# Kernel optimization log

Measured on AMD Instinct MI355X. Metric: run time of the kernel, lower is better.

## Reference

```python
import jax, jax.numpy as jnp
import numpy as np

SHORT_LEN = 10
NEG_INF = -1.0e9


def _attn_pool(values, user, w, w_bias, extra_b, mask, softmax_axis):
    # values: [B,L,D], user: [B,D]; linear+bias+relu, dot with user, masked softmax, weighted sum
    h = jax.nn.relu(jnp.einsum('bld,ed->ble', values, w) + w_bias + extra_b)
    s = jnp.einsum('bld,bd->bl', h, user)
    s = jnp.where(mask, NEG_INF, s)
    a = jax.nn.softmax(s, axis=softmax_axis)
    return jnp.einsum('bld,bl->bd', values, a)


def setup_inputs() -> dict:
    key = jax.random.key(0)
    ks = jax.random.split(key, 10)
    B, L, D, NI, NU = 2048, 50, 64, 100000, 100000
    return {
        'seq': jax.random.randint(ks[0], (B, L), 0, NI),
        'user_id': jax.random.randint(ks[1], (B,), 0, NU),
        'item_emb': jax.random.normal(ks[2], (NI, D), jnp.float32) * 0.01,
        'user_emb': jax.random.normal(ks[3], (NU, D), jnp.float32) * 0.01,
        'long_w': jax.random.normal(ks[4], (D, D), jnp.float32) * 0.1,
        'long_w_bias': jax.random.normal(ks[5], (D,), jnp.float32) * 0.1,
        'long_b': jax.random.normal(ks[6], (D,), jnp.float32) * 0.1,
        'long_short_w': jax.random.normal(ks[7], (D, D), jnp.float32) * 0.1,
        'long_short_w_bias': jax.random.normal(ks[8], (D,), jnp.float32) * 0.1,
        'long_short_b': jax.random.normal(ks[9], (D,), jnp.float32) * 0.1,
    }


def reference(seq, user_id, item_emb, user_emb, long_w, long_w_bias, long_b,
              long_short_w, long_short_w_bias, long_short_b):
    e = item_emb[seq]                     # [B,L,D]
    u = user_emb[user_id]                 # [B,D]
    mask = seq == 0                       # padding mask
    # long-term attention pooling (softmax over dim=1)
    long_term = _attn_pool(e, u, long_w, long_w_bias, long_b, mask, 1)[:, None, :]  # [B,1,D]
    # concat long-term summary with last SHORT_LEN items
    short = e[:, -SHORT_LEN:, :]
    mask_ls = jnp.concatenate([jnp.zeros((seq.shape[0], 1), bool), mask[:, -SHORT_LEN:]], axis=1)
    ls = jnp.concatenate([long_term, short], axis=1)  # [B,1+K,D]
    pooled = _attn_pool(ls, u, long_short_w, long_short_w_bias, long_short_b, mask_ls, -1)  # [B,D]
    scores = pooled @ item_emb.T          # [B, n_items]
    return scores
```

## Files before the change

kernel.cpp:

```cpp
#include <hip/hip_runtime.h>
#include <hip/hip_bf16.h>


#define L_SEQ 50
#define D_EMB 64
#define SHORT_LEN 10
#define LS_LEN 11
#define NEG_INF_F (-1000000000.0f)

typedef __bf16 bf16x8 __attribute__((ext_vector_type(8)));
typedef float f32x4 __attribute__((ext_vector_type(4)));

__device__ __forceinline__ float wave_sum(float v) {
#pragma unroll
  for (int off = 32; off > 0; off >>= 1) v += __shfl_xor(v, off, 64);
  return v;
}
__device__ __forceinline__ float wave_max(float v) {
#pragma unroll
  for (int off = 32; off > 0; off >>= 1) v = fmaxf(v, __shfl_xor(v, off, 64));
  return v;
}

__global__ __launch_bounds__(64) void pool_kernel(
    const int* __restrict__ seq, const int* __restrict__ user_id,
    const float* __restrict__ item_emb, const float* __restrict__ user_emb,
    const float* __restrict__ w1, const float* __restrict__ w1b, const float* __restrict__ b1,
    const float* __restrict__ w2, const float* __restrict__ w2b, const float* __restrict__ b2,
    float* __restrict__ pooled_f32, __bf16* __restrict__ pooled_bf) {
  const int b = blockIdx.x;
  const int lane = threadIdx.x;

  __shared__ float e_lds[L_SEQ][D_EMB];
  __shared__ float ls_lds[LS_LEN][D_EMB];
  __shared__ float a_lds[D_EMB];
  __shared__ int seq_lds[L_SEQ];

  if (lane < L_SEQ) seq_lds[lane] = seq[b * L_SEQ + lane];
  const float u = user_emb[(long)user_id[b] * D_EMB + lane];
  __syncthreads();

  for (int l = 0; l < L_SEQ; ++l) {
    e_lds[l][lane] = item_emb[(long)seq_lds[l] * D_EMB + lane];
  }

  float4 w1r[16];
#pragma unroll
  for (int k = 0; k < 16; ++k) w1r[k] = *(const float4*)&w1[lane * D_EMB + 4 * k];
  const float bias1 = w1b[lane] + b1[lane];
  __syncthreads();

  float s_val = 0.0f;
  for (int l = 0; l < L_SEQ; ++l) {
    float acc = bias1;
#pragma unroll
    for (int k = 0; k < 16; ++k) {
      float4 ev = *(const float4*)&e_lds[l][4 * k];
      acc = fmaf(ev.x, w1r[k].x, acc);
      acc = fmaf(ev.y, w1r[k].y, acc);
      acc = fmaf(ev.z, w1r[k].z, acc);
      acc = fmaf(ev.w, w1r[k].w, acc);
    }
    acc = fmaxf(acc, 0.0f);
    float t = wave_sum(acc * u);
    if (lane == l) s_val = (seq_lds[l] == 0) ? NEG_INF_F : t;
  }
  {
    float x = (lane < L_SEQ) ? s_val : -INFINITY;
    float m = wave_max(x);
    float p = (lane < L_SEQ) ? __expf(x - m) : 0.0f;
    float ps = wave_sum(p);
    a_lds[lane] = p / ps;
  }
  __syncthreads();

  float lt = 0.0f;
  for (int l = 0; l < L_SEQ; ++l) lt = fmaf(a_lds[l], e_lds[l][lane], lt);
  __syncthreads();

  ls_lds[0][lane] = lt;
#pragma unroll
  for (int j = 1; j < LS_LEN; ++j)
    ls_lds[j][lane] = e_lds[L_SEQ - SHORT_LEN + (j - 1)][lane];

  float4 w2r[16];
#pragma unroll
  for (int k = 0; k < 16; ++k) w2r[k] = *(const float4*)&w2[lane * D_EMB + 4 * k];
  const float bias2 = w2b[lane] + b2[lane];
  __syncthreads();

  float s2_val = 0.0f;
  for (int j = 0; j < LS_LEN; ++j) {
    float acc = bias2;
#pragma unroll
    for (int k = 0; k < 16; ++k) {
      float4 lv = *(const float4*)&ls_lds[j][4 * k];
      acc = fmaf(lv.x, w2r[k].x, acc);
      acc = fmaf(lv.y, w2r[k].y, acc);
      acc = fmaf(lv.z, w2r[k].z, acc);
      acc = fmaf(lv.w, w2r[k].w, acc);
    }
    acc = fmaxf(acc, 0.0f);
    float t = wave_sum(acc * u);
    bool msk = (j == 0) ? false : (seq_lds[L_SEQ - SHORT_LEN + (j - 1)] == 0);
    if (lane == j) s2_val = msk ? NEG_INF_F : t;
  }
  {
    float x = (lane < LS_LEN) ? s2_val : -INFINITY;
    float m = wave_max(x);
    float p = (lane < LS_LEN) ? __expf(x - m) : 0.0f;
    float ps = wave_sum(p);
    __syncthreads();
    a_lds[lane] = p / ps;
  }
  __syncthreads();

  float po = 0.0f;
#pragma unroll
  for (int j = 0; j < LS_LEN; ++j) po = fmaf(a_lds[j], ls_lds[j][lane], po);
  if (pooled_f32) pooled_f32[(long)b * D_EMB + lane] = po;
  if (pooled_bf) pooled_bf[(long)b * D_EMB + lane] = (__bf16)po;
}

__global__ __launch_bounds__(256) void cvt_bf16_kernel(
    const float* __restrict__ in, __bf16* __restrict__ out, int n8) {
  int i = blockIdx.x * blockDim.x + threadIdx.x;
  if (i >= n8) return;
  float4 a = ((const float4*)in)[2 * i];
  float4 b = ((const float4*)in)[2 * i + 1];
  bf16x8 v;
  v[0] = (__bf16)a.x; v[1] = (__bf16)a.y; v[2] = (__bf16)a.z; v[3] = (__bf16)a.w;
  v[4] = (__bf16)b.x; v[5] = (__bf16)b.y; v[6] = (__bf16)b.z; v[7] = (__bf16)b.w;
  ((bf16x8*)out)[i] = v;
}

__global__ __launch_bounds__(256) void scores_mfma_kernel(
    const __bf16* __restrict__ pooled_bf,
    const __bf16* __restrict__ item_bf,
    float* __restrict__ out, int NI, int n_tiles) {
  const int tid = threadIdx.x;
  const int w = tid >> 6;
  const int l = tid & 63;
  const int lr = l & 15;
  const int lg = l >> 4;
  const int b0 = blockIdx.x * 64;

  bf16x8 afrag[4][2];
#pragma unroll
  for (int g = 0; g < 4; ++g) {
    const __bf16* arow = pooled_bf + (size_t)(b0 + 16 * g + lr) * D_EMB + 8 * lg;
    afrag[g][0] = *(const bf16x8*)(arow);
    afrag[g][1] = *(const bf16x8*)(arow + 32);
  }

  const int t0 = blockIdx.y * 32;
  for (int tl = w; tl < 32; tl += 4) {
    const int t = t0 + tl;
    if (t >= n_tiles) break;
    const __bf16* brow = item_bf + (size_t)(t * 16 + lr) * D_EMB + 8 * lg;
    bf16x8 bf0 = *(const bf16x8*)(brow);
    bf16x8 bf1 = *(const bf16x8*)(brow + 32);
#pragma unroll
    for (int g = 0; g < 4; ++g) {
      f32x4 acc = {0.f, 0.f, 0.f, 0.f};
      acc = __builtin_amdgcn_mfma_f32_16x16x32_bf16(afrag[g][0], bf0, acc, 0, 0, 0);
      acc = __builtin_amdgcn_mfma_f32_16x16x32_bf16(afrag[g][1], bf1, acc, 0, 0, 0);
      float* orow = out + (size_t)(b0 + 16 * g + 4 * lg) * NI + t * 16 + lr;
#pragma unroll
      for (int r = 0; r < 4; ++r) orow[(size_t)r * NI] = acc[r];
    }
  }
}

__global__ __launch_bounds__(256) void scores_kernel(
    const float* __restrict__ pooled, const float* __restrict__ item_emb,
    float* __restrict__ out, int NI) {
  constexpr int STR = 68;
  __shared__ __align__(16) float poolT[64 * STR];
  __shared__ __align__(16) float itemT[64 * STR];

  const int tid = threadIdx.x;
  const int lane = tid & 63;
  const int b0 = blockIdx.x * 64;
  const int i0 = blockIdx.y * 64;

  for (int r = tid >> 6; r < 64; r += 4) {
    poolT[lane * STR + r] = pooled[(long)(b0 + r) * D_EMB + lane];
    int i = i0 + r;
    itemT[lane * STR + r] = (i < NI) ? item_emb[(long)i * D_EMB + lane] : 0.0f;
  }
  __syncthreads();

  const int tx = tid & 15;
  const int ty = tid >> 4;
  float acc[4][4] = {};

#pragma unroll 8
  for (int d = 0; d < 64; ++d) {
    float4 pv = *(const float4*)&poolT[d * STR + ty * 4];
    float4 iv = *(const float4*)&itemT[d * STR + tx * 4];
    float pva[4] = {pv.x, pv.y, pv.z, pv.w};
    float iva[4] = {iv.x, iv.y, iv.z, iv.w};
#pragma unroll
    for (int m = 0; m < 4; ++m)
#pragma unroll
      for (int n = 0; n < 4; ++n) acc[m][n] = fmaf(pva[m], iva[n], acc[m][n]);
  }

  const int ibase = i0 + tx * 4;
  const long orow = (long)(b0 + ty * 4);
  if (i0 + 63 < NI) {
#pragma unroll
    for (int m = 0; m < 4; ++m) {
      float4 v = make_float4(acc[m][0], acc[m][1], acc[m][2], acc[m][3]);
      *(float4*)&out[(orow + m) * (long)NI + ibase] = v;
    }
  } else {
#pragma unroll
    for (int m = 0; m < 4; ++m)
#pragma unroll
      for (int n = 0; n < 4; ++n)
        if (ibase + n < NI) out[(orow + m) * (long)NI + ibase + n] = acc[m][n];
  }
}

extern "C" void kernel_launch(void* const* d_in, const int* in_sizes, int n_in,
                              void* d_out, int out_size, void* d_ws, size_t ws_size,
                              hipStream_t stream) {
  const int* seq = (const int*)d_in[0];
  const int* user_id = (const int*)d_in[1];
  const float* item_emb = (const float*)d_in[2];
  const float* user_emb = (const float*)d_in[3];
  const float* w1 = (const float*)d_in[4];
  const float* w1b = (const float*)d_in[5];
  const float* b1 = (const float*)d_in[6];
  const float* w2 = (const float*)d_in[7];
  const float* w2b = (const float*)d_in[8];
  const float* b2 = (const float*)d_in[9];
  float* out = (float*)d_out;

  const int B = in_sizes[1];
  const int NI = in_sizes[2] / D_EMB;

  const size_t item_bf_bytes = (size_t)NI * D_EMB * 2;
  const size_t pooled_bf_bytes = (size_t)B * D_EMB * 2;
  const bool mfma_ok = (ws_size >= item_bf_bytes + pooled_bf_bytes) &&
                       (NI % 16 == 0) && (B % 64 == 0) && (D_EMB == 64);

  if (mfma_ok) {
    __bf16* item_bf = (__bf16*)d_ws;
    __bf16* pooled_bf = (__bf16*)((char*)d_ws + item_bf_bytes);

    const int n8 = NI * D_EMB / 8;
    cvt_bf16_kernel<<<(n8 + 255) / 256, 256, 0, stream>>>(item_emb, item_bf, n8);

    pool_kernel<<<B, 64, 0, stream>>>(seq, user_id, item_emb, user_emb,
                                      w1, w1b, b1, w2, w2b, b2,
                                      (float*)nullptr, pooled_bf);

    const int n_tiles = NI / 16;
    dim3 grid(B / 64, (n_tiles + 31) / 32);
    scores_mfma_kernel<<<grid, 256, 0, stream>>>(pooled_bf, item_bf, out, NI, n_tiles);
  } else {
    float* pooled = (float*)d_ws;
    pool_kernel<<<B, 64, 0, stream>>>(seq, user_id, item_emb, user_emb,
                                      w1, w1b, b1, w2, w2b, b2,
                                      pooled, (__bf16*)nullptr);
    dim3 grid(B / 64, (NI + 63) / 64);
    scores_kernel<<<grid, 256, 0, stream>>>(pooled, item_emb, out, NI);
  }
}
```

Measured before the change: 313.0 us.

## Fuse item bf16 conversion into scores MFMA kernel and vectorize output stores

Removes the separate fp32-to-bf16 conversion pass over the item table and converts item rows in registers inside the scores kernel. The MFMA operands are swapped so each lane holds four consecutive item columns, which allows float4 output stores instead of scalar strided stores. The grid is remapped so each block covers 256 batch rows (64 per wave) over a strip of 64 item tiles. The cost is that every block reads fp32 item data, so the item table is fetched at twice the width and converted 8 times across batch blocks instead of once.

```diff
diff --git a/kernel.cpp b/kernel.cpp
--- a/kernel.cpp
+++ b/kernel.cpp
@@ -7,6 +7,7 @@
 #define SHORT_LEN 10
 #define LS_LEN 11
 #define NEG_INF_F (-1000000000.0f)
+#define TILE_STRIP 64
 
 typedef __bf16 bf16x8 __attribute__((ext_vector_type(8)));
 typedef float f32x4 __attribute__((ext_vector_type(4)));
@@ -122,52 +123,52 @@
   if (pooled_bf) pooled_bf[(long)b * D_EMB + lane] = (__bf16)po;
 }
 
-__global__ __launch_bounds__(256) void cvt_bf16_kernel(
-    const float* __restrict__ in, __bf16* __restrict__ out, int n8) {
-  int i = blockIdx.x * blockDim.x + threadIdx.x;
-  if (i >= n8) return;
-  float4 a = ((const float4*)in)[2 * i];
-  float4 b = ((const float4*)in)[2 * i + 1];
+__device__ __forceinline__ bf16x8 cvt_bf8(float4 a, float4 b) {
   bf16x8 v;
   v[0] = (__bf16)a.x; v[1] = (__bf16)a.y; v[2] = (__bf16)a.z; v[3] = (__bf16)a.w;
   v[4] = (__bf16)b.x; v[5] = (__bf16)b.y; v[6] = (__bf16)b.z; v[7] = (__bf16)b.w;
-  ((bf16x8*)out)[i] = v;
+  return v;
 }
 
 __global__ __launch_bounds__(256) void scores_mfma_kernel(
     const __bf16* __restrict__ pooled_bf,
-    const __bf16* __restrict__ item_bf,
+    const float* __restrict__ item_emb,
     float* __restrict__ out, int NI, int n_tiles) {
   const int tid = threadIdx.x;
   const int w = tid >> 6;
   const int l = tid & 63;
   const int lr = l & 15;
   const int lg = l >> 4;
-  const int b0 = blockIdx.x * 64;
-
-  bf16x8 afrag[4][2];
+  const int b0 = blockIdx.y * 256 + w * 64;
+
+  bf16x8 pfrag[4][2];
 #pragma unroll
   for (int g = 0; g < 4; ++g) {
-    const __bf16* arow = pooled_bf + (size_t)(b0 + 16 * g + lr) * D_EMB + 8 * lg;
-    afrag[g][0] = *(const bf16x8*)(arow);
-    afrag[g][1] = *(const bf16x8*)(arow + 32);
-  }
-
-  const int t0 = blockIdx.y * 32;
-  for (int tl = w; tl < 32; tl += 4) {
-    const int t = t0 + tl;
-    if (t >= n_tiles) break;
-    const __bf16* brow = item_bf + (size_t)(t * 16 + lr) * D_EMB + 8 * lg;
-    bf16x8 bf0 = *(const bf16x8*)(brow);
-    bf16x8 bf1 = *(const bf16x8*)(brow + 32);
+    const __bf16* prow = pooled_bf + (size_t)(b0 + 16 * g + lr) * D_EMB + 8 * lg;
+    pfrag[g][0] = *(const bf16x8*)(prow);
+    pfrag[g][1] = *(const bf16x8*)(prow + 32);
+  }
+
+  const int t_begin = blockIdx.x * TILE_STRIP;
+  const int t_end = min(t_begin + TILE_STRIP, n_tiles);
+
+#pragma unroll 2
+  for (int t = t_begin; t < t_end; ++t) {
+    const float* irow = item_emb + (size_t)(t * 16 + lr) * D_EMB + 8 * lg;
+    float4 i0 = *(const float4*)(irow);
+    float4 i1 = *(const float4*)(irow + 4);
+    float4 i2 = *(const float4*)(irow + 32);
+    float4 i3 = *(const float4*)(irow + 36);
+    bf16x8 a0 = cvt_bf8(i0, i1);
+    bf16x8 a1 = cvt_bf8(i2, i3);
+
 #pragma unroll
     for (int g = 0; g < 4; ++g) {
       f32x4 acc = {0.f, 0.f, 0.f, 0.f};
-      acc = __builtin_amdgcn_mfma_f32_16x16x32_bf16(afrag[g][0], bf0, acc, 0, 0, 0);
-      acc = __builtin_amdgcn_mfma_f32_16x16x32_bf16(afrag[g][1], bf1, acc, 0, 0, 0);
-      float* orow = out + (size_t)(b0 + 16 * g + 4 * lg) * NI + t * 16 + lr;
-#pragma unroll
-      for (int r = 0; r < 4; ++r) orow[(size_t)r * NI] = acc[r];
+      acc = __builtin_amdgcn_mfma_f32_16x16x32_bf16(a0, pfrag[g][0], acc, 0, 0, 0);
+      acc = __builtin_amdgcn_mfma_f32_16x16x32_bf16(a1, pfrag[g][1], acc, 0, 0, 0);
+      float* op = out + (size_t)(b0 + 16 * g + lr) * NI + t * 16 + 4 * lg;
+      *(float4*)op = make_float4(acc[0], acc[1], acc[2], acc[3]);
     }
   }
 }
@@ -242,25 +243,20 @@
   const int B = in_sizes[1];
   const int NI = in_sizes[2] / D_EMB;
 
-  const size_t item_bf_bytes = (size_t)NI * D_EMB * 2;
   const size_t pooled_bf_bytes = (size_t)B * D_EMB * 2;
-  const bool mfma_ok = (ws_size >= item_bf_bytes + pooled_bf_bytes) &&
-                       (NI % 16 == 0) && (B % 64 == 0) && (D_EMB == 64);
+  const bool mfma_ok = (ws_size >= pooled_bf_bytes) &&
+                       (NI % 16 == 0) && (B % 256 == 0) && (D_EMB == 64);
 
   if (mfma_ok) {
-    __bf16* item_bf = (__bf16*)d_ws;
-    __bf16* pooled_bf = (__bf16*)((char*)d_ws + item_bf_bytes);
-
-    const int n8 = NI * D_EMB / 8;
-    cvt_bf16_kernel<<<(n8 + 255) / 256, 256, 0, stream>>>(item_emb, item_bf, n8);
+    __bf16* pooled_bf = (__bf16*)d_ws;
 
     pool_kernel<<<B, 64, 0, stream>>>(seq, user_id, item_emb, user_emb,
                                       w1, w1b, b1, w2, w2b, b2,
                                       (float*)nullptr, pooled_bf);
 
     const int n_tiles = NI / 16;
-    dim3 grid(B / 64, (n_tiles + 31) / 32);
-    scores_mfma_kernel<<<grid, 256, 0, stream>>>(pooled_bf, item_bf, out, NI, n_tiles);
+    dim3 grid((n_tiles + TILE_STRIP - 1) / TILE_STRIP, B / 256);
+    scores_mfma_kernel<<<grid, 256, 0, stream>>>(pooled_bf, item_emb, out, NI, n_tiles);
   } else {
     float* pooled = (float*)d_ws;
     pool_kernel<<<B, 64, 0, stream>>>(seq, user_id, item_emb, user_emb,
```

New measurement: 420.4 us. +34.3%, slower.
